# Optimization experiments

Hardware: AMD Instinct MI355X
Metric: run time of the kernel (lower is better)

Reference implementation:

```python
import jax, jax.numpy as jnp
import numpy as np

B, F, D_IN, D_K, D_V = 4, 4096, 1024, 128, 128


def setup_inputs() -> dict:
    key = jax.random.key(0)
    ks = jax.random.split(key, 7)
    s_in = 1.0 / np.sqrt(D_IN)
    x = jax.random.normal(ks[0], (B, F, D_IN), dtype=jnp.float32)
    # nn.Linear weights stored as (out, in); we keep (in, out) for x @ W
    Wq = jax.random.uniform(ks[1], (D_IN, D_K), jnp.float32, -s_in, s_in)
    bq = jax.random.uniform(ks[2], (D_K,), jnp.float32, -s_in, s_in)
    Wk = jax.random.uniform(ks[3], (D_IN, D_K), jnp.float32, -s_in, s_in)
    bk = jax.random.uniform(ks[4], (D_K,), jnp.float32, -s_in, s_in)
    Wv = jax.random.uniform(ks[5], (D_IN, D_V), jnp.float32, -s_in, s_in)
    bv = jax.random.uniform(ks[6], (D_V,), jnp.float32, -s_in, s_in)
    return {"x": x, "Wq": Wq, "bq": bq, "Wk": Wk, "bk": bk, "Wv": Wv, "bv": bv}


def reference(x, Wq, bq, Wk, bk, Wv, bv):
    Q = x @ Wq + bq  # (B, F, d_k)
    K = x @ Wk + bk  # (B, F, d_k)
    V = x @ Wv + bv  # (B, F, d_v)
    scale = 1.0 / jnp.sqrt(jnp.asarray(Q.shape[-1], Q.dtype))
    scores = jnp.einsum('bqd,bkd->bqk', Q, K) * scale  # (B, F, F)
    attn = jax.nn.softmax(scores, axis=-1)
    return jnp.einsum('bqk,bkd->bqd', attn, V)  # (B, F, d_v)
```

## Files before the change

kernel.cpp:

```cpp
#include <hip/hip_runtime.h>

#define TB 4
#define TF 4096
#define DIN 1024
#define DK 128
#define M_TOT (TB * TF)

typedef __attribute__((ext_vector_type(8))) short sh8;
typedef __attribute__((ext_vector_type(4))) float f32x4;

#if __has_builtin(__builtin_amdgcn_exp2f)
#define EXP2(x) __builtin_amdgcn_exp2f(x)
#else
#define EXP2(x) exp2f(x)
#endif

__device__ __forceinline__ unsigned short f2bf(float f) {
  unsigned int u = __builtin_bit_cast(unsigned int, f);
  u += 0x7FFFu + ((u >> 16) & 1u);
  return (unsigned short)(u >> 16);
}

__device__ __forceinline__ unsigned int pack_bf2(float a, float b) {
  return (unsigned int)f2bf(a) | ((unsigned int)f2bf(b) << 16);
}

__device__ __forceinline__ float bf2f(unsigned short u) {
  unsigned int x = ((unsigned int)u) << 16;
  return __builtin_bit_cast(float, x);
}

__global__ __launch_bounds__(256) void prep_wt_kernel(
    const float* __restrict__ Wq, const float* __restrict__ Wk,
    const float* __restrict__ Wv, unsigned short* __restrict__ Wf) {
  int idx = blockIdx.x * 256 + threadIdx.x;
  int j = idx & 7;
  int lane = (idx >> 3) & 63;
  int ks = (idx >> 9) & 31;
  int t = (idx >> 14) & 7;
  int p = idx >> 17;
  int col = t * 16 + (lane & 15);
  int k = ks * 32 + (lane >> 4) * 8 + j;
  const float* W = (p == 0) ? Wq : (p == 1) ? Wk : Wv;
  Wf[idx] = f2bf(W[k * DK + col]);
}

__global__ __launch_bounds__(512, 2) void proj_kernel(
    const float* __restrict__ x,
    const unsigned short* __restrict__ Wf,
    const float* __restrict__ bq, const float* __restrict__ bk,
    const float* __restrict__ bv,
    unsigned short* __restrict__ Qb,
    unsigned short* __restrict__ Kb,
    unsigned short* __restrict__ VT)
{
  const int tid = threadIdx.x;
  const int wave = tid >> 6;
  const int lane = tid & 63;
  const int lr = lane & 15;
  const int lg = lane >> 4;
  const int m0 = blockIdx.x * 64;
  const int col = wave * 16 + lr;

  __shared__ unsigned short Xlds[64 * 68];

  f32x4 acc[3][4];
  const f32x4 z4 = {0.f, 0.f, 0.f, 0.f};
#pragma unroll
  for (int p = 0; p < 3; ++p)
#pragma unroll
    for (int m = 0; m < 4; ++m) acc[p][m] = z4;

  const int xr = tid >> 3;
  const int xk8 = (tid & 7) * 8;

  for (int k0 = 0; k0 < DIN; k0 += 64) {
    const float* xp = x + (size_t)(m0 + xr) * DIN + k0 + xk8;
    const float4 f0 = *(const float4*)xp;
    const float4 f1 = *(const float4*)(xp + 4);
    union { sh8 v; unsigned short u[8]; } U;
    U.u[0] = f2bf(f0.x); U.u[1] = f2bf(f0.y);
    U.u[2] = f2bf(f0.z); U.u[3] = f2bf(f0.w);
    U.u[4] = f2bf(f1.x); U.u[5] = f2bf(f1.y);
    U.u[6] = f2bf(f1.z); U.u[7] = f2bf(f1.w);
    __syncthreads();
    *(sh8*)&Xlds[xr * 68 + xk8] = U.v;
    __syncthreads();

    sh8 a[4][2];
#pragma unroll
    for (int m = 0; m < 4; ++m)
#pragma unroll
      for (int s = 0; s < 2; ++s)
        a[m][s] = *(const sh8*)&Xlds[(m * 16 + lr) * 68 + s * 32 + lg * 8];
#pragma unroll
    for (int p = 0; p < 3; ++p) {
#pragma unroll
      for (int s = 0; s < 2; ++s) {
        sh8 b = *(const sh8*)(Wf +
                              ((size_t)((p * 8 + wave) * 32 + (k0 >> 5) + s)) *
                                  512 +
                              lane * 8);
#pragma unroll
        for (int m = 0; m < 4; ++m)
          acc[p][m] = __builtin_amdgcn_mfma_f32_16x16x32_bf16(a[m][s], b,
                                                              acc[p][m], 0, 0,
                                                              0);
      }
    }
  }

  const float scale = 0.12751744f;
  const int b_idx = m0 >> 12;
  const float add_q = bq[col];
  const float add_k = bk[col];
  const float add_v = bv[col];
#pragma unroll
  for (int m = 0; m < 4; ++m) {
    const int rowbase = m0 + m * 16 + lg * 4;
#pragma unroll
    for (int r = 0; r < 4; ++r) {
      Qb[(size_t)(rowbase + r) * DK + col] =
          f2bf((acc[0][m][r] + add_q) * scale);
      Kb[(size_t)(rowbase + r) * DK + col] = f2bf(acc[1][m][r] + add_k);
    }
    const int fbase = (m0 & (TF - 1)) + m * 16 + lg * 4;
    ushort4 pv;
    pv.x = f2bf(acc[2][m][0] + add_v);
    pv.y = f2bf(acc[2][m][1] + add_v);
    pv.z = f2bf(acc[2][m][2] + add_v);
    pv.w = f2bf(acc[2][m][3] + add_v);
    *(ushort4*)(VT + ((size_t)b_idx * DK + col) * TF + fbase) = pv;
  }
}

template <int SPLIT>
__global__ __launch_bounds__(512, 2) void attn_part_kernel(
    const unsigned short* __restrict__ Qb, const unsigned short* __restrict__ Kb,
    const unsigned short* __restrict__ VT, unsigned short* __restrict__ Opart,
    float* __restrict__ Mpart, float* __restrict__ Lpart,
    float* __restrict__ out) {
  constexpr int CHUNK = TF / SPLIT;
  const int tid = threadIdx.x;
  const int lane = tid & 63;
  const int lr = lane & 15;
  const int lg = lane >> 4;

  const int bid = blockIdx.x;
  const int xcd = bid & 7;
  const int batch = xcd >> 1;
  const int idb = ((bid >> 3) << 1) | (xcd & 1);
  const int slot = idb / SPLIT;
  const int chunk = idb % SPLIT;
  const int wave = tid >> 6;
  const int q0 = batch * TF + slot * 128 + wave * 16;
  const int kbase = chunk * CHUNK;

  __shared__ unsigned short Klds[64 * 136];
  __shared__ unsigned short Vlds[128 * 72];

  const unsigned short* Qp = Qb + (size_t)q0 * DK;
  const unsigned short* Kp = Kb + (size_t)batch * TF * DK;
  const unsigned short* Vp = VT + (size_t)batch * DK * TF;

  sh8 aq[4];
#pragma unroll
  for (int dd = 0; dd < 4; ++dd)
    aq[dd] = *(const sh8*)(Qp + lr * DK + dd * 32 + lg * 8);

  const f32x4 z4 = {0.f, 0.f, 0.f, 0.f};
  f32x4 ot[8];
#pragma unroll
  for (int nb = 0; nb < 8; ++nb) ot[nb] = z4;
  float mrow = -1e30f, lrow = 0.f;

  const int srcA = lr + ((lane >> 4) & 1) * 32;
  const int srcB = srcA + 16;
  const bool chi = (lg >= 2);

  for (int kk0 = kbase; kk0 < kbase + CHUNK; kk0 += 64) {
    __syncthreads();
#pragma unroll
    for (int i = 0; i < 2; ++i) {
      int c = tid + i * 512;
      int row = c >> 4, c8 = c & 15;
      *(uint4*)&Klds[row * 136 + c8 * 8] =
          *(const uint4*)(Kp + (size_t)(kk0 + row) * DK + c8 * 8);
    }
#pragma unroll
    for (int i = 0; i < 2; ++i) {
      int c = tid + i * 512;
      int row = c >> 3, c8 = c & 7;
      *(uint4*)&Vlds[row * 72 + c8 * 8] =
          *(const uint4*)(Vp + (size_t)row * TF + kk0 + c8 * 8);
    }
    __syncthreads();

    f32x4 st[4];
#pragma unroll
    for (int c = 0; c < 4; ++c) st[c] = z4;
#pragma unroll
    for (int dd = 0; dd < 4; ++dd) {
#pragma unroll
      for (int c = 0; c < 4; ++c) {
        sh8 kb = *(const sh8*)&Klds[(c * 16 + lr) * 136 + dd * 32 + lg * 8];
        st[c] =
            __builtin_amdgcn_mfma_f32_16x16x32_bf16(kb, aq[dd], st[c], 0, 0, 0);
      }
    }

    float mx = st[0][0];
#pragma unroll
    for (int c = 0; c < 4; ++c)
#pragma unroll
      for (int r = 0; r < 4; ++r) mx = fmaxf(mx, st[c][r]);
    mx = fmaxf(mx, __shfl_xor(mx, 16));
    mx = fmaxf(mx, __shfl_xor(mx, 32));

    if (!__all(mx - mrow <= 11.5f)) {
      const float mnew = fmaxf(mrow, mx);
      const float al = EXP2(mrow - mnew);
      lrow *= al;
#pragma unroll
      for (int nb = 0; nb < 8; ++nb)
#pragma unroll
        for (int r = 0; r < 4; ++r) ot[nb][r] *= al;
      mrow = mnew;
    }

    float p[4][4];
    float rs = 0.f;
#pragma unroll
    for (int c = 0; c < 4; ++c)
#pragma unroll
      for (int r = 0; r < 4; ++r) {
        p[c][r] = EXP2(st[c][r] - mrow);
        rs += p[c][r];
      }
    rs += __shfl_xor(rs, 16);
    rs += __shfl_xor(rs, 32);
    lrow += rs;

    unsigned int up[4][2];
#pragma unroll
    for (int c = 0; c < 4; ++c) {
      up[c][0] = pack_bf2(p[c][0], p[c][1]);
      up[c][1] = pack_bf2(p[c][2], p[c][3]);
    }

#pragma unroll
    for (int ks = 0; ks < 2; ++ks) {
      unsigned int e0 = __shfl((int)up[2 * ks][0], srcA);
      unsigned int o0 = __shfl((int)up[2 * ks + 1][0], srcA);
      unsigned int e1 = __shfl((int)up[2 * ks][1], srcA);
      unsigned int o1 = __shfl((int)up[2 * ks + 1][1], srcA);
      unsigned int e2 = __shfl((int)up[2 * ks][0], srcB);
      unsigned int o2 = __shfl((int)up[2 * ks + 1][0], srcB);
      unsigned int e3 = __shfl((int)up[2 * ks][1], srcB);
      unsigned int o3 = __shfl((int)up[2 * ks + 1][1], srcB);
      union { unsigned int u[4]; sh8 v; } PA;
      PA.u[0] = chi ? o0 : e0;
      PA.u[1] = chi ? o1 : e1;
      PA.u[2] = chi ? o2 : e2;
      PA.u[3] = chi ? o3 : e3;
#pragma unroll
      for (int nb = 0; nb < 8; ++nb) {
        sh8 vb = *(const sh8*)&Vlds[(nb * 16 + lr) * 72 + ks * 32 + lg * 8];
        ot[nb] =
            __builtin_amdgcn_mfma_f32_16x16x32_bf16(vb, PA.v, ot[nb], 0, 0, 0);
      }
    }
  }

  if constexpr (SPLIT == 1) {
    const float inv = 1.0f / lrow;
#pragma unroll
    for (int nb = 0; nb < 8; ++nb) {
      float4 res = {ot[nb][0] * inv, ot[nb][1] * inv, ot[nb][2] * inv,
                    ot[nb][3] * inv};
      *(float4*)(out + (size_t)(q0 + lr) * DK + nb * 16 + lg * 4) = res;
    }
  } else {
    const int row = q0 + lr;
    if (lg == 0) {
      Mpart[(size_t)chunk * M_TOT + row] = mrow;
      Lpart[(size_t)chunk * M_TOT + row] = lrow;
    }
#pragma unroll
    for (int nb = 0; nb < 8; ++nb) {
      ushort4 res;
      res.x = f2bf(ot[nb][0]); res.y = f2bf(ot[nb][1]);
      res.z = f2bf(ot[nb][2]); res.w = f2bf(ot[nb][3]);
      *(ushort4*)(Opart + ((size_t)chunk * M_TOT + row) * DK + nb * 16 +
                  lg * 4) = res;
    }
  }
}

__global__ __launch_bounds__(256) void combine_kernel(
    const unsigned short* __restrict__ Opart, const float* __restrict__ Mpart,
    const float* __restrict__ Lpart, float* __restrict__ out, int split) {
  const int idx = blockIdx.x * 256 + threadIdx.x;
  const int row = idx >> 5;
  const int cq = (idx & 31) << 2;
  float m = -1e30f;
  for (int s = 0; s < split; ++s) m = fmaxf(m, Mpart[(size_t)s * M_TOT + row]);
  float den = 0.f;
  float4 acc = {0.f, 0.f, 0.f, 0.f};
  for (int s = 0; s < split; ++s) {
    const float w = EXP2(Mpart[(size_t)s * M_TOT + row] - m);
    den += w * Lpart[(size_t)s * M_TOT + row];
    const ushort4 v =
        *(const ushort4*)(Opart + ((size_t)s * M_TOT + row) * DK + cq);
    acc.x += w * bf2f(v.x); acc.y += w * bf2f(v.y);
    acc.z += w * bf2f(v.z); acc.w += w * bf2f(v.w);
  }
  const float inv = 1.0f / den;
  float4 res = {acc.x * inv, acc.y * inv, acc.z * inv, acc.w * inv};
  *(float4*)(out + (size_t)row * DK + cq) = res;
}

extern "C" void kernel_launch(void* const* d_in, const int* in_sizes, int n_in,
                              void* d_out, int out_size, void* d_ws,
                              size_t ws_size, hipStream_t stream) {
  const float* x = (const float*)d_in[0];
  const float* Wq = (const float*)d_in[1];
  const float* bq = (const float*)d_in[2];
  const float* Wk = (const float*)d_in[3];
  const float* bk = (const float*)d_in[4];
  const float* Wv = (const float*)d_in[5];
  const float* bv = (const float*)d_in[6];
  float* out = (float*)d_out;

  unsigned short* Wf = (unsigned short*)d_ws;
  unsigned short* Qb = Wf + 3 * DK * DIN;
  unsigned short* Kb = Qb + (size_t)M_TOT * DK;
  unsigned short* VT = Kb + (size_t)M_TOT * DK;
  unsigned short* Opart = VT + (size_t)M_TOT * DK;
  const size_t base_bytes = 2ull * (3 * DK * DIN + 3ull * M_TOT * DK);
  const size_t per_split = (size_t)M_TOT * DK * 2 + 2ull * M_TOT * 4;

  prep_wt_kernel<<<(3 * DK * DIN) / 256, 256, 0, stream>>>(Wq, Wk, Wv, Wf);
  proj_kernel<<<M_TOT / 64, 512, 0, stream>>>(x, Wf, bq, bk, bv, Qb, Kb, VT);

  int split;
  if (ws_size >= base_bytes + 4 * per_split) split = 4;
  else if (ws_size >= base_bytes + 2 * per_split) split = 2;
  else split = 1;

  float* Mpart = (float*)(Opart + (size_t)split * M_TOT * DK);
  float* Lpart = Mpart + (size_t)split * M_TOT;

  if (split == 4) {
    attn_part_kernel<4><<<128 * 4, 512, 0, stream>>>(Qb, Kb, VT, Opart, Mpart,
                                                     Lpart, out);
    combine_kernel<<<M_TOT * 32 / 256, 256, 0, stream>>>(Opart, Mpart, Lpart,
                                                         out, 4);
  } else if (split == 2) {
    attn_part_kernel<2><<<128 * 2, 512, 0, stream>>>(Qb, Kb, VT, Opart, Mpart,
                                                     Lpart, out);
    combine_kernel<<<M_TOT * 32 / 256, 256, 0, stream>>>(Opart, Mpart, Lpart,
                                                         out, 2);
  } else {
    attn_part_kernel<1><<<128, 512, 0, stream>>>(Qb, Kb, VT, nullptr, nullptr,
                                                 nullptr, out);
  }
}
```

Baseline: 104.6 us.

## Double-buffer K/V tiles in LDS for attention partial kernel

```diff
diff --git a/kernel.cpp b/kernel.cpp
--- a/kernel.cpp
+++ b/kernel.cpp
@@ -141,6 +141,7 @@
     float* __restrict__ Mpart, float* __restrict__ Lpart,
     float* __restrict__ out) {
   constexpr int CHUNK = TF / SPLIT;
+  constexpr int NT = CHUNK / 64;
   const int tid = threadIdx.x;
   const int lane = tid & 63;
   const int lr = lane & 15;
@@ -156,13 +157,16 @@
   const int q0 = batch * TF + slot * 128 + wave * 16;
   const int kbase = chunk * CHUNK;
 
-  __shared__ unsigned short Klds[64 * 136];
-  __shared__ unsigned short Vlds[128 * 72];
+  __shared__ unsigned short Klds[2][64 * 136];
+  __shared__ unsigned short Vlds[2][128 * 72];
 
   const unsigned short* Qp = Qb + (size_t)q0 * DK;
   const unsigned short* Kp = Kb + (size_t)batch * TF * DK;
   const unsigned short* Vp = VT + (size_t)batch * DK * TF;
 
+  const int krow0 = tid >> 4, kc8 = tid & 15;
+  const int vrow0 = tid >> 3, vc8 = tid & 7;
+
   sh8 aq[4];
 #pragma unroll
   for (int dd = 0; dd < 4; ++dd)
@@ -178,23 +182,30 @@
   const int srcB = srcA + 16;
   const bool chi = (lg >= 2);
 
-  for (int kk0 = kbase; kk0 < kbase + CHUNK; kk0 += 64) {
-    __syncthreads();
-#pragma unroll
-    for (int i = 0; i < 2; ++i) {
-      int c = tid + i * 512;
-      int row = c >> 4, c8 = c & 15;
-      *(uint4*)&Klds[row * 136 + c8 * 8] =
-          *(const uint4*)(Kp + (size_t)(kk0 + row) * DK + c8 * 8);
-    }
-#pragma unroll
-    for (int i = 0; i < 2; ++i) {
-      int c = tid + i * 512;
-      int row = c >> 3, c8 = c & 7;
-      *(uint4*)&Vlds[row * 72 + c8 * 8] =
-          *(const uint4*)(Vp + (size_t)row * TF + kk0 + c8 * 8);
-    }
-    __syncthreads();
+#pragma unroll
+  for (int i = 0; i < 2; ++i) {
+    *(uint4*)&Klds[0][(krow0 + i * 32) * 136 + kc8 * 8] =
+        *(const uint4*)(Kp + (size_t)(kbase + krow0 + i * 32) * DK + kc8 * 8);
+    *(uint4*)&Vlds[0][(vrow0 + i * 64) * 72 + vc8 * 8] =
+        *(const uint4*)(Vp + (size_t)(vrow0 + i * 64) * TF + kbase + vc8 * 8);
+  }
+  __syncthreads();
+
+  for (int t = 0; t < NT; ++t) {
+    const int kk0 = kbase + t * 64;
+    const int cur = t & 1;
+
+    if (t + 1 < NT) {
+#pragma unroll
+      for (int i = 0; i < 2; ++i) {
+        *(uint4*)&Klds[cur ^ 1][(krow0 + i * 32) * 136 + kc8 * 8] =
+            *(const uint4*)(Kp + (size_t)(kk0 + 64 + krow0 + i * 32) * DK +
+                            kc8 * 8);
+        *(uint4*)&Vlds[cur ^ 1][(vrow0 + i * 64) * 72 + vc8 * 8] =
+            *(const uint4*)(Vp + (size_t)(vrow0 + i * 64) * TF + kk0 + 64 +
+                            vc8 * 8);
+      }
+    }
 
     f32x4 st[4];
 #pragma unroll
@@ -203,7 +214,8 @@
     for (int dd = 0; dd < 4; ++dd) {
 #pragma unroll
       for (int c = 0; c < 4; ++c) {
-        sh8 kb = *(const sh8*)&Klds[(c * 16 + lr) * 136 + dd * 32 + lg * 8];
+        sh8 kb =
+            *(const sh8*)&Klds[cur][(c * 16 + lr) * 136 + dd * 32 + lg * 8];
         st[c] =
             __builtin_amdgcn_mfma_f32_16x16x32_bf16(kb, aq[dd], st[c], 0, 0, 0);
       }
@@ -265,11 +277,14 @@
       PA.u[3] = chi ? o3 : e3;
 #pragma unroll
       for (int nb = 0; nb < 8; ++nb) {
-        sh8 vb = *(const sh8*)&Vlds[(nb * 16 + lr) * 72 + ks * 32 + lg * 8];
+        sh8 vb =
+            *(const sh8*)&Vlds[cur][(nb * 16 + lr) * 72 + ks * 32 + lg * 8];
         ot[nb] =
             __builtin_amdgcn_mfma_f32_16x16x32_bf16(vb, PA.v, ot[nb], 0, 0, 0);
       }
     }
+
+    __syncthreads();
   }
 
   if constexpr (SPLIT == 1) {
```

Result: no change. 104.7 us (+0.1%).
